# Kernel tuning notes

Measured on AMD Instinct MI355X. Metric: run time of the kernel, lower is better.

The kernel has to match this reference:

```python
import jax, jax.numpy as jnp
import numpy as np

H = 224 * 224  # hardcoded histogram length in the original module


def _fill_hist(h_prev, c):
    """Faithful vectorization of the per-row python range-fill.

    Original loop semantics with boundaries c[0..N-1] (ints via truncation):
      j=0:        h[0 : c[0]]        = 0
      0<j<N-1:    h[c[j-1] : c[j]]   = j
      j=N-1:      h[c[N-1] : ]       = N-1
    Note the region [c[N-2], c[N-1]) is NEVER written at this call, so it
    retains the stale value from the previous channel (a bug we preserve).
    For pixel p outside that stale gap, the value is exactly
    searchsorted(c[:N-1], p, side='right').
    """
    ci = jnp.clip(c.astype(jnp.int32), 0, H)  # int() truncation + slice clamp
    N = ci.shape[0]
    p = jnp.arange(H, dtype=jnp.int32)
    j = jnp.searchsorted(ci[: N - 1], p, side='right').astype(h_prev.dtype)
    stale = (p >= ci[N - 2]) & (p < ci[N - 1])
    return jnp.where(stale, h_prev, j)


def setup_inputs() -> dict:
    key = jax.random.key(0)
    k1, k2 = jax.random.split(key)
    N = 8192  # number of histogram bins per channel
    scale = H / (N * 0.5)  # so E[cumsum total] ~= H = 50176
    target = jax.random.uniform(k1, (3, N, 1), dtype=jnp.float32) * scale
    output = jax.random.uniform(k2, (3, N, 1), dtype=jnp.float32) * scale
    return {"target": target, "output": output}


def reference(target, output):
    # h1/h2 persist across the 3 channel iterations (module state, init zeros)
    h1 = jnp.zeros(H, dtype=jnp.float32)
    h2 = jnp.zeros(H, dtype=jnp.float32)
    loss = jnp.asarray(0.0, dtype=jnp.float32)
    for i in range(3):  # fixed small channel loop, as in the original
        c1 = jnp.cumsum(target[i, :, 0])
        c2 = jnp.cumsum(output[i, :, 0])
        h1 = _fill_hist(h1, c1)
        h2 = _fill_hist(h2, c2)
        loss = loss + jnp.sqrt(jnp.sum(jnp.square(h1 - h2)))
    return loss
```

## Files before the change

### kernel.cpp

```cpp
#include <hip/hip_runtime.h>
#include <math.h>


#define H_TOT 50176
#define NBIN  8192
#define NPAD  (NBIN + 2)
#define NBLK  98
#define NTHR  512
#define SLOT  16
#define WS_NEEDED (NBLK * SLOT * 8)

#define CVT(x) ((unsigned short)min(max((int)(x), 0), H_TOT))

__global__ __launch_bounds__(NTHR)
void l2hist_part(const float* __restrict__ target,
                 const float* __restrict__ output,
                 unsigned long long* __restrict__ ws)
{
    __shared__ unsigned short lci[6][NPAD];
    __shared__ unsigned long long red[3][NTHR / 64];

    const int tid  = threadIdx.x;
    const int lane = tid & 63;
    const int wave = tid >> 6;

    if (wave < 6) {
        const float* base = (wave < 3) ? (target + wave * NBIN)
                                       : (output + (wave - 3) * NBIN);
        unsigned short* dst = lci[wave];
        float running = 0.f;
        for (int t = 0; t < 16; t += 2) {
            const float* up = base + t * 512 + 8 * lane;
            const float* wp = base + (t + 1) * 512 + 8 * lane;
            float4 ua = *reinterpret_cast<const float4*>(up);
            float4 ub = *reinterpret_cast<const float4*>(up + 4);
            float4 wa = *reinterpret_cast<const float4*>(wp);
            float4 wb = *reinterpret_cast<const float4*>(wp + 4);
            const float u1 = ua.x + ua.y, u2 = u1 + ua.z, u3 = u2 + ua.w;
            const float u4 = u3 + ub.x, u5 = u4 + ub.y, u6 = u5 + ub.z, u7 = u6 + ub.w;
            const float w1 = wa.x + wa.y, w2 = w1 + wa.z, w3 = w2 + wa.w;
            const float w4 = w3 + wb.x, w5 = w4 + wb.y, w6 = w5 + wb.z, w7 = w6 + wb.w;
            float su = u7, sw = w7;
            #pragma unroll
            for (int d = 1; d < 64; d <<= 1) {
                float au = __shfl_up(su, d);
                float aw = __shfl_up(sw, d);
                if (lane >= d) { su += au; sw += aw; }
            }
            const float totu = __shfl(su, 63);
            const float totw = __shfl(sw, 63);
            const float bu = running + (su - u7);
            const float bw = running + totu + (sw - w7);
            running += totu + totw;

            ushort4 o;
            unsigned short* du = dst + t * 512 + 8 * lane;
            o.x = CVT(bu + ua.x); o.y = CVT(bu + u1);
            o.z = CVT(bu + u2);   o.w = CVT(bu + u3);
            *reinterpret_cast<ushort4*>(du) = o;
            o.x = CVT(bu + u4);   o.y = CVT(bu + u5);
            o.z = CVT(bu + u6);   o.w = CVT(bu + u7);
            *reinterpret_cast<ushort4*>(du + 4) = o;

            unsigned short* dw = dst + (t + 1) * 512 + 8 * lane;
            o.x = CVT(bw + wa.x); o.y = CVT(bw + w1);
            o.z = CVT(bw + w2);   o.w = CVT(bw + w3);
            *reinterpret_cast<ushort4*>(dw) = o;
            o.x = CVT(bw + w4);   o.y = CVT(bw + w5);
            o.z = CVT(bw + w6);   o.w = CVT(bw + w7);
            *reinterpret_cast<ushort4*>(dw + 4) = o;
        }
    }
    __syncthreads();

    const int p = blockIdx.x * NTHR + tid;

    int lo[6], hi[6];
    #pragma unroll
    for (int a = 0; a < 6; ++a) { lo[a] = 0; hi[a] = NBIN - 1; }
    #pragma unroll
    for (int it = 0; it < 13; ++it) {
        #pragma unroll
        for (int a = 0; a < 6; ++a) {
            int mid = (lo[a] + hi[a]) >> 1;
            int c   = (int)lci[a][mid];
            bool go = (lo[a] < hi[a]);
            bool le = (c <= p);
            lo[a] = go ? (le ? mid + 1 : lo[a]) : lo[a];
            hi[a] = go ? (le ? hi[a]  : mid)    : hi[a];
        }
    }

    int a0, a1, a2, b0, b1, b2;
    {
        int e00 = lci[0][NBIN - 2], e10 = lci[0][NBIN - 1];
        int e01 = lci[1][NBIN - 2], e11 = lci[1][NBIN - 1];
        int e02 = lci[2][NBIN - 2], e12 = lci[2][NBIN - 1];
        int e03 = lci[3][NBIN - 2], e13 = lci[3][NBIN - 1];
        int e04 = lci[4][NBIN - 2], e14 = lci[4][NBIN - 1];
        int e05 = lci[5][NBIN - 2], e15 = lci[5][NBIN - 1];
        a0 = (p >= e00 && p < e10) ? 0  : lo[0];
        a1 = (p >= e01 && p < e11) ? a0 : lo[1];
        a2 = (p >= e02 && p < e12) ? a1 : lo[2];
        b0 = (p >= e03 && p < e13) ? 0  : lo[3];
        b1 = (p >= e04 && p < e14) ? b0 : lo[4];
        b2 = (p >= e05 && p < e15) ? b1 : lo[5];
    }
    const int d0 = a0 - b0, d1 = a1 - b1, d2 = a2 - b2;
    unsigned long long s0 = (unsigned long long)(d0 * d0);
    unsigned long long s1 = (unsigned long long)(d1 * d1);
    unsigned long long s2 = (unsigned long long)(d2 * d2);

    #pragma unroll
    for (int d = 32; d > 0; d >>= 1) {
        s0 += __shfl_down(s0, d);
        s1 += __shfl_down(s1, d);
        s2 += __shfl_down(s2, d);
    }
    if (lane == 0) { red[0][wave] = s0; red[1][wave] = s1; red[2][wave] = s2; }
    __syncthreads();

    if (tid == 0) {
        unsigned long long S0 = 0, S1 = 0, S2 = 0;
        #pragma unroll
        for (int w = 0; w < NTHR / 64; ++w) {
            S0 += red[0][w]; S1 += red[1][w]; S2 += red[2][w];
        }
        unsigned long long* slot = ws + (size_t)blockIdx.x * SLOT;
        slot[0] = S0;
        slot[1] = S1;
        slot[2] = S2;
    }
}

__global__ __launch_bounds__(64)
void l2hist_final(const unsigned long long* __restrict__ ws,
                  float* __restrict__ out)
{
    const int lane = threadIdx.x;
    unsigned long long s0 = 0, s1 = 0, s2 = 0;
    for (int s = lane; s < NBLK; s += 64) {
        const unsigned long long* slot = ws + (size_t)s * SLOT;
        s0 += slot[0]; s1 += slot[1]; s2 += slot[2];
    }
    #pragma unroll
    for (int d = 32; d > 0; d >>= 1) {
        s0 += __shfl_down(s0, d);
        s1 += __shfl_down(s1, d);
        s2 += __shfl_down(s2, d);
    }
    if (lane == 0)
        out[0] = sqrtf((float)s0) + sqrtf((float)s1) + sqrtf((float)s2);
}

#define FB_THREADS 1024
#define FB_PPT 49

__global__ __launch_bounds__(FB_THREADS)
void l2hist_fallback(const float* __restrict__ target,
                     const float* __restrict__ output,
                     float* __restrict__ out)
{
    __shared__ unsigned short ci[6][NBIN];
    __shared__ float red[3][FB_THREADS / 64];

    const int tid  = threadIdx.x;
    const int lane = tid & 63;
    const int wave = tid >> 6;

    if (wave < 6) {
        const float* src = ((wave < 3) ? (target + wave * NBIN)
                                       : (output + (wave - 3) * NBIN)) + lane * 128;
        float s = 0.f;
        #pragma unroll
        for (int t = 0; t < 32; ++t) {
            float4 v = reinterpret_cast<const float4*>(src)[t];
            s += (v.x + v.y) + (v.z + v.w);
        }
        float x = s;
        #pragma unroll
        for (int d = 1; d < 64; d <<= 1) {
            float y = __shfl_up(x, d);
            if (lane >= d) x += y;
        }
        float run = x - s;
        unsigned short* dst = ci[wave] + lane * 128;
        #pragma unroll
        for (int t = 0; t < 32; ++t) {
            float4 v = reinterpret_cast<const float4*>(src)[t];
            run += v.x; int q0 = (int)run;
            run += v.y; int q1 = (int)run;
            run += v.z; int q2 = (int)run;
            run += v.w; int q3 = (int)run;
            dst[t * 4 + 0] = (unsigned short)min(max(q0, 0), H_TOT);
            dst[t * 4 + 1] = (unsigned short)min(max(q1, 0), H_TOT);
            dst[t * 4 + 2] = (unsigned short)min(max(q2, 0), H_TOT);
            dst[t * 4 + 3] = (unsigned short)min(max(q3, 0), H_TOT);
        }
    }
    __syncthreads();

    int e0[6], e1[6];
    #pragma unroll
    for (int a = 0; a < 6; ++a) {
        e0[a] = (int)ci[a][NBIN - 2];
        e1[a] = (int)ci[a][NBIN - 1];
    }
    const int p0 = tid * FB_PPT;
    int jj[6], cur[6];
    #pragma unroll
    for (int a = 0; a < 6; ++a) {
        int lo = 0, hi = NBIN - 1;
        while (lo < hi) {
            int mid = (lo + hi) >> 1;
            if ((int)ci[a][mid] < p0) lo = mid + 1; else hi = mid;
        }
        jj[a]  = lo;
        cur[a] = (lo < NBIN - 1) ? (int)ci[a][lo] : 0x7FFFFFFF;
    }
    float s0 = 0.f, s1 = 0.f, s2 = 0.f;
    for (int t = 0; t < FB_PPT; ++t) {
        const int p = p0 + t;
        int v[6];
        #pragma unroll
        for (int a = 0; a < 6; ++a) {
            while (cur[a] <= p) {
                ++jj[a];
                cur[a] = (jj[a] < NBIN - 1) ? (int)ci[a][jj[a]] : 0x7FFFFFFF;
            }
            v[a] = jj[a];
        }
        const int a0 = (p >= e0[0] && p < e1[0]) ? 0  : v[0];
        const int a1 = (p >= e0[1] && p < e1[1]) ? a0 : v[1];
        const int a2 = (p >= e0[2] && p < e1[2]) ? a1 : v[2];
        const int b0 = (p >= e0[3] && p < e1[3]) ? 0  : v[3];
        const int b1 = (p >= e0[4] && p < e1[4]) ? b0 : v[4];
        const int b2 = (p >= e0[5] && p < e1[5]) ? b1 : v[5];
        const float d0 = (float)(a0 - b0);
        const float d1 = (float)(a1 - b1);
        const float d2 = (float)(a2 - b2);
        s0 = fmaf(d0, d0, s0);
        s1 = fmaf(d1, d1, s1);
        s2 = fmaf(d2, d2, s2);
    }
    #pragma unroll
    for (int d = 32; d > 0; d >>= 1) {
        s0 += __shfl_down(s0, d);
        s1 += __shfl_down(s1, d);
        s2 += __shfl_down(s2, d);
    }
    if (lane == 0) { red[0][wave] = s0; red[1][wave] = s1; red[2][wave] = s2; }
    __syncthreads();
    if (tid == 0) {
        float S0 = 0.f, S1 = 0.f, S2 = 0.f;
        #pragma unroll
        for (int w = 0; w < FB_THREADS / 64; ++w) {
            S0 += red[0][w]; S1 += red[1][w]; S2 += red[2][w];
        }
        out[0] = sqrtf(S0) + sqrtf(S1) + sqrtf(S2);
    }
}

extern "C" void kernel_launch(void* const* d_in, const int* in_sizes, int n_in,
                              void* d_out, int out_size, void* d_ws, size_t ws_size,
                              hipStream_t stream)
{
    const float* target = (const float*)d_in[0];
    const float* output = (const float*)d_in[1];
    float* out = (float*)d_out;

    if (ws_size < (size_t)WS_NEEDED) {
        l2hist_fallback<<<dim3(1), dim3(FB_THREADS), 0, stream>>>(target, output, out);
        return;
    }
    unsigned long long* ws = (unsigned long long*)d_ws;
    l2hist_part<<<dim3(NBLK), dim3(NTHR), 0, stream>>>(target, output, ws);
    l2hist_final<<<dim3(1), dim3(64), 0, stream>>>(ws, out);
}
```

Baseline: 21.81 us.

## Share binary search across pixel pairs and widen cumsum unroll to four segments

The prefix-sum phase now processes four 512-element segments per iteration instead of two, interleaving four wave-level shuffle scans to expose more ILP. The lookup phase has half the threads each handle two adjacent pixels. A thread binary-searches once for the first pixel and finds the second by linear stepping from that result, which roughly halves the shared-memory binary-search loads. The cost is that half of each block's threads sit idle in the search phase, and the linear walk is data-dependent and divergent when many boundaries equal p1.

```diff
diff --git a/kernel.cpp b/kernel.cpp
--- a/kernel.cpp
+++ b/kernel.cpp
@@ -25,91 +25,148 @@
     const int wave = tid >> 6;
 
     if (wave < 6) {
-        const float* base = (wave < 3) ? (target + wave * NBIN)
-                                       : (output + (wave - 3) * NBIN);
+        const float* basep = (wave < 3) ? (target + wave * NBIN)
+                                        : (output + (wave - 3) * NBIN);
         unsigned short* dst = lci[wave];
         float running = 0.f;
-        for (int t = 0; t < 16; t += 2) {
-            const float* up = base + t * 512 + 8 * lane;
-            const float* wp = base + (t + 1) * 512 + 8 * lane;
-            float4 ua = *reinterpret_cast<const float4*>(up);
-            float4 ub = *reinterpret_cast<const float4*>(up + 4);
-            float4 wa = *reinterpret_cast<const float4*>(wp);
-            float4 wb = *reinterpret_cast<const float4*>(wp + 4);
-            const float u1 = ua.x + ua.y, u2 = u1 + ua.z, u3 = u2 + ua.w;
-            const float u4 = u3 + ub.x, u5 = u4 + ub.y, u6 = u5 + ub.z, u7 = u6 + ub.w;
-            const float w1 = wa.x + wa.y, w2 = w1 + wa.z, w3 = w2 + wa.w;
-            const float w4 = w3 + wb.x, w5 = w4 + wb.y, w6 = w5 + wb.z, w7 = w6 + wb.w;
-            float su = u7, sw = w7;
+        for (int t = 0; t < 16; t += 4) {
+            const float* sp0 = basep + (t + 0) * 512 + 8 * lane;
+            const float* sp1 = basep + (t + 1) * 512 + 8 * lane;
+            const float* sp2 = basep + (t + 2) * 512 + 8 * lane;
+            const float* sp3 = basep + (t + 3) * 512 + 8 * lane;
+            float4 A0 = *reinterpret_cast<const float4*>(sp0);
+            float4 B0 = *reinterpret_cast<const float4*>(sp0 + 4);
+            float4 A1 = *reinterpret_cast<const float4*>(sp1);
+            float4 B1 = *reinterpret_cast<const float4*>(sp1 + 4);
+            float4 A2 = *reinterpret_cast<const float4*>(sp2);
+            float4 B2 = *reinterpret_cast<const float4*>(sp2 + 4);
+            float4 A3 = *reinterpret_cast<const float4*>(sp3);
+            float4 B3 = *reinterpret_cast<const float4*>(sp3 + 4);
+
+            const float a1 = A0.x + A0.y, a2 = a1 + A0.z, a3 = a2 + A0.w;
+            const float a4 = a3 + B0.x, a5 = a4 + B0.y, a6 = a5 + B0.z, a7 = a6 + B0.w;
+            const float b1 = A1.x + A1.y, b2 = b1 + A1.z, b3 = b2 + A1.w;
+            const float b4 = b3 + B1.x, b5 = b4 + B1.y, b6 = b5 + B1.z, b7 = b6 + B1.w;
+            const float c1 = A2.x + A2.y, c2 = c1 + A2.z, c3 = c2 + A2.w;
+            const float c4 = c3 + B2.x, c5 = c4 + B2.y, c6 = c5 + B2.z, c7 = c6 + B2.w;
+            const float d1 = A3.x + A3.y, d2 = d1 + A3.z, d3 = d2 + A3.w;
+            const float d4 = d3 + B3.x, d5 = d4 + B3.y, d6 = d5 + B3.z, d7 = d6 + B3.w;
+
+            float s0 = a7, s1 = b7, s2 = c7, s3 = d7;
             #pragma unroll
             for (int d = 1; d < 64; d <<= 1) {
-                float au = __shfl_up(su, d);
-                float aw = __shfl_up(sw, d);
-                if (lane >= d) { su += au; sw += aw; }
+                float t0 = __shfl_up(s0, d);
+                float t1 = __shfl_up(s1, d);
+                float t2 = __shfl_up(s2, d);
+                float t3 = __shfl_up(s3, d);
+                if (lane >= d) { s0 += t0; s1 += t1; s2 += t2; s3 += t3; }
             }
-            const float totu = __shfl(su, 63);
-            const float totw = __shfl(sw, 63);
-            const float bu = running + (su - u7);
-            const float bw = running + totu + (sw - w7);
-            running += totu + totw;
+            const float T0 = __shfl(s0, 63), T1 = __shfl(s1, 63);
+            const float T2 = __shfl(s2, 63), T3 = __shfl(s3, 63);
+            const float base0 = running + (s0 - a7);
+            const float base1 = running + T0 + (s1 - b7);
+            const float base2 = running + T0 + T1 + (s2 - c7);
+            const float base3 = running + T0 + T1 + T2 + (s3 - d7);
+            running += T0 + T1 + T2 + T3;
 
             ushort4 o;
-            unsigned short* du = dst + t * 512 + 8 * lane;
-            o.x = CVT(bu + ua.x); o.y = CVT(bu + u1);
-            o.z = CVT(bu + u2);   o.w = CVT(bu + u3);
-            *reinterpret_cast<ushort4*>(du) = o;
-            o.x = CVT(bu + u4);   o.y = CVT(bu + u5);
-            o.z = CVT(bu + u6);   o.w = CVT(bu + u7);
-            *reinterpret_cast<ushort4*>(du + 4) = o;
-
-            unsigned short* dw = dst + (t + 1) * 512 + 8 * lane;
-            o.x = CVT(bw + wa.x); o.y = CVT(bw + w1);
-            o.z = CVT(bw + w2);   o.w = CVT(bw + w3);
-            *reinterpret_cast<ushort4*>(dw) = o;
-            o.x = CVT(bw + w4);   o.y = CVT(bw + w5);
-            o.z = CVT(bw + w6);   o.w = CVT(bw + w7);
-            *reinterpret_cast<ushort4*>(dw + 4) = o;
+            unsigned short* d0p = dst + (t + 0) * 512 + 8 * lane;
+            o.x = CVT(base0 + A0.x); o.y = CVT(base0 + a1);
+            o.z = CVT(base0 + a2);   o.w = CVT(base0 + a3);
+            *reinterpret_cast<ushort4*>(d0p) = o;
+            o.x = CVT(base0 + a4);   o.y = CVT(base0 + a5);
+            o.z = CVT(base0 + a6);   o.w = CVT(base0 + a7);
+            *reinterpret_cast<ushort4*>(d0p + 4) = o;
+
+            unsigned short* d1p = dst + (t + 1) * 512 + 8 * lane;
+            o.x = CVT(base1 + A1.x); o.y = CVT(base1 + b1);
+            o.z = CVT(base1 + b2);   o.w = CVT(base1 + b3);
+            *reinterpret_cast<ushort4*>(d1p) = o;
+            o.x = CVT(base1 + b4);   o.y = CVT(base1 + b5);
+            o.z = CVT(base1 + b6);   o.w = CVT(base1 + b7);
+            *reinterpret_cast<ushort4*>(d1p + 4) = o;
+
+            unsigned short* d2p = dst + (t + 2) * 512 + 8 * lane;
+            o.x = CVT(base2 + A2.x); o.y = CVT(base2 + c1);
+            o.z = CVT(base2 + c2);   o.w = CVT(base2 + c3);
+            *reinterpret_cast<ushort4*>(d2p) = o;
+            o.x = CVT(base2 + c4);   o.y = CVT(base2 + c5);
+            o.z = CVT(base2 + c6);   o.w = CVT(base2 + c7);
+            *reinterpret_cast<ushort4*>(d2p + 4) = o;
+
+            unsigned short* d3p = dst + (t + 3) * 512 + 8 * lane;
+            o.x = CVT(base3 + A3.x); o.y = CVT(base3 + d1);
+            o.z = CVT(base3 + d2);   o.w = CVT(base3 + d3);
+            *reinterpret_cast<ushort4*>(d3p) = o;
+            o.x = CVT(base3 + d4);   o.y = CVT(base3 + d5);
+            o.z = CVT(base3 + d6);   o.w = CVT(base3 + d7);
+            *reinterpret_cast<ushort4*>(d3p + 4) = o;
         }
     }
     __syncthreads();
 
-    const int p = blockIdx.x * NTHR + tid;
-
-    int lo[6], hi[6];
-    #pragma unroll
-    for (int a = 0; a < 6; ++a) { lo[a] = 0; hi[a] = NBIN - 1; }
-    #pragma unroll
-    for (int it = 0; it < 13; ++it) {
+    unsigned long long s0 = 0, s1 = 0, s2 = 0;
+    if (tid < 256) {
+        const int p0 = blockIdx.x * NTHR + 2 * tid;
+        const int p1 = p0 + 1;
+
+        int lo[6], hi[6];
+        #pragma unroll
+        for (int a = 0; a < 6; ++a) { lo[a] = 0; hi[a] = NBIN - 1; }
+        #pragma unroll
+        for (int it = 0; it < 13; ++it) {
+            #pragma unroll
+            for (int a = 0; a < 6; ++a) {
+                int mid = (lo[a] + hi[a]) >> 1;
+                int c   = (int)lci[a][mid];
+                bool go = (lo[a] < hi[a]);
+                bool le = (c <= p0);
+                lo[a] = go ? (le ? mid + 1 : lo[a]) : lo[a];
+                hi[a] = go ? (le ? hi[a]  : mid)    : hi[a];
+            }
+        }
+        int v1[6];
         #pragma unroll
         for (int a = 0; a < 6; ++a) {
-            int mid = (lo[a] + hi[a]) >> 1;
-            int c   = (int)lci[a][mid];
-            bool go = (lo[a] < hi[a]);
-            bool le = (c <= p);
-            lo[a] = go ? (le ? mid + 1 : lo[a]) : lo[a];
-            hi[a] = go ? (le ? hi[a]  : mid)    : hi[a];
-        }
-    }
-
-    int a0, a1, a2, b0, b1, b2;
-    {
+            int j = lo[a];
+            while (j < NBIN - 1 && (int)lci[a][j] <= p1) ++j;
+            v1[a] = j;
+        }
+
         int e00 = lci[0][NBIN - 2], e10 = lci[0][NBIN - 1];
         int e01 = lci[1][NBIN - 2], e11 = lci[1][NBIN - 1];
         int e02 = lci[2][NBIN - 2], e12 = lci[2][NBIN - 1];
         int e03 = lci[3][NBIN - 2], e13 = lci[3][NBIN - 1];
         int e04 = lci[4][NBIN - 2], e14 = lci[4][NBIN - 1];
         int e05 = lci[5][NBIN - 2], e15 = lci[5][NBIN - 1];
-        a0 = (p >= e00 && p < e10) ? 0  : lo[0];
-        a1 = (p >= e01 && p < e11) ? a0 : lo[1];
-        a2 = (p >= e02 && p < e12) ? a1 : lo[2];
-        b0 = (p >= e03 && p < e13) ? 0  : lo[3];
-        b1 = (p >= e04 && p < e14) ? b0 : lo[4];
-        b2 = (p >= e05 && p < e15) ? b1 : lo[5];
-    }
-    const int d0 = a0 - b0, d1 = a1 - b1, d2 = a2 - b2;
-    unsigned long long s0 = (unsigned long long)(d0 * d0);
-    unsigned long long s1 = (unsigned long long)(d1 * d1);
-    unsigned long long s2 = (unsigned long long)(d2 * d2);
+
+        {
+            const int p = p0;
+            int x0 = (p >= e00 && p < e10) ? 0  : lo[0];
+            int x1 = (p >= e01 && p < e11) ? x0 : lo[1];
+            int x2 = (p >= e02 && p < e12) ? x1 : lo[2];
+            int y0 = (p >= e03 && p < e13) ? 0  : lo[3];
+            int y1 = (p >= e04 && p < e14) ? y0 : lo[4];
+            int y2 = (p >= e05 && p < e15) ? y1 : lo[5];
+            const int q0 = x0 - y0, q1 = x1 - y1, q2 = x2 - y2;
+            s0 += (unsigned long long)(q0 * q0);
+            s1 += (unsigned long long)(q1 * q1);
+            s2 += (unsigned long long)(q2 * q2);
+        }
+        {
+            const int p = p1;
+            int x0 = (p >= e00 && p < e10) ? 0  : v1[0];
+            int x1 = (p >= e01 && p < e11) ? x0 : v1[1];
+            int x2 = (p >= e02 && p < e12) ? x1 : v1[2];
+            int y0 = (p >= e03 && p < e13) ? 0  : v1[3];
+            int y1 = (p >= e04 && p < e14) ? y0 : v1[4];
+            int y2 = (p >= e05 && p < e15) ? y1 : v1[5];
+            const int q0 = x0 - y0, q1 = x1 - y1, q2 = x2 - y2;
+            s0 += (unsigned long long)(q0 * q0);
+            s1 += (unsigned long long)(q1 * q1);
+            s2 += (unsigned long long)(q2 * q2);
+        }
+    }
 
     #pragma unroll
     for (int d = 32; d > 0; d >>= 1) {
```

After: 21.52 us. No clear change (-1.3%).
